# Performance work log

Hardware: AMD Instinct MI355X
Metric: run time of the kernel (lower is better)

Reference implementation:

```python
import jax, jax.numpy as jnp
import numpy as np

DIM = 512
HEADS = 8
DIM_HEAD = 64
INNER = HEADS * DIM_HEAD  # 512
LN_EPS = 1e-5


def setup_inputs() -> dict:
    key = jax.random.key(0)
    ks = jax.random.split(key, 6)
    b, n = 2, 2048
    x = jax.random.normal(ks[0], (b, n, DIM), dtype=jnp.float32)
    # to_qkv: Linear(dim, inner*3, bias=False); torch weight is [out,in], apply as x @ W.T
    w_qkv = jax.random.normal(ks[1], (3 * INNER, DIM), dtype=jnp.float32) * (DIM ** -0.5)
    reattn_w = jax.random.normal(ks[2], (HEADS, HEADS), dtype=jnp.float32)
    ln_g = jnp.ones((HEADS,), dtype=jnp.float32)
    ln_b = jnp.zeros((HEADS,), dtype=jnp.float32)
    w_out = jax.random.normal(ks[3], (DIM, INNER), dtype=jnp.float32) * (INNER ** -0.5)
    b_out = jnp.zeros((DIM,), dtype=jnp.float32)
    return {"x": x, "w_qkv": w_qkv, "reattn_w": reattn_w,
            "ln_g": ln_g, "ln_b": ln_b, "w_out": w_out, "b_out": b_out}


def reference(x, w_qkv, reattn_w, ln_g, ln_b, w_out, b_out):
    b, n, _ = x.shape
    scale = DIM_HEAD ** -0.5
    qkv = x @ w_qkv.T  # [b, n, 3*inner]
    q, k, v = jnp.split(qkv, 3, axis=-1)
    # b n (h d) -> b h n d
    split_heads = lambda t: t.reshape(b, n, HEADS, DIM_HEAD).transpose(0, 2, 1, 3)
    q, k, v = split_heads(q), split_heads(k), split_heads(v)
    dots = jnp.einsum('bhid,bhjd->bhij', q, k) * scale
    attn = jax.nn.softmax(dots, axis=-1)
    # re-attention: cross-head mixing then LayerNorm over head dim
    attn = jnp.einsum('bhij,hg->bgij', attn, reattn_w)
    a = attn.transpose(0, 2, 3, 1)  # b i j h
    mu = jnp.mean(a, axis=-1, keepdims=True)
    var = jnp.mean((a - mu) ** 2, axis=-1, keepdims=True)
    a = (a - mu) * jax.lax.rsqrt(var + LN_EPS) * ln_g + ln_b
    attn = a.transpose(0, 3, 1, 2)  # b h i j
    out = jnp.einsum('bhij,bhjd->bhid', attn, v)
    out = out.transpose(0, 2, 1, 3).reshape(b, n, INNER)
    out = out @ w_out.T + b_out  # dropout p=0 -> identity
    return out
```

## Files before the change

### kernel.cpp

```cpp
#include <hip/hip_runtime.h>
#include <hip/hip_bf16.h>


typedef __attribute__((ext_vector_type(8))) short bfx8;
typedef __attribute__((ext_vector_type(4))) float f32x4;
typedef unsigned short u16;
typedef unsigned int u32;

#define QSCALE 0.18033688011112042f

static __device__ inline u16 f2bf(float f) {
  union { float f; unsigned u; } cv; cv.f = f;
  unsigned u = cv.u;
  u += 0x7fffu + ((u >> 16) & 1u);
  return (u16)(u >> 16);
}
static __device__ inline u32 cvtpk(float lo, float hi) {
  u32 d; asm("v_cvt_pk_bf16_f32 %0, %1, %2" : "=v"(d) : "v"(lo), "v"(hi)); return d;
}
static __device__ inline float fexp2(float x) {
  float r; asm("v_exp_f32 %0, %1" : "=v"(r) : "v"(x)); return r;
}
static __device__ inline float flog2(float x) {
  float r; asm("v_log_f32 %0, %1" : "=v"(r) : "v"(x)); return r;
}
static __device__ inline uint4 pk8(const float* p) {
  float4 a = *(const float4*)p, b = *(const float4*)(p + 4);
  return make_uint4(cvtpk(a.x, a.y), cvtpk(a.z, a.w), cvtpk(b.x, b.y), cvtpk(b.z, b.w));
}

__global__ __launch_bounds__(256) void gemm_qkv(
    const float* __restrict__ A, const float* __restrict__ B,
    u16* __restrict__ qb, u16* __restrict__ kb, u16* __restrict__ vtb) {
  __shared__ u16 As[128 * 32];
  __shared__ u16 Bs[128 * 32];
  const int bid = blockIdx.x;
  const int swzb = (bid & 7) * 48 + (bid >> 3);
  const int n0 = (swzb % 12) * 128, m0 = (swzb / 12) * 128;
  const int t = threadIdx.x, lane = t & 63;
  const int wm = (t >> 6) >> 1, wn = (t >> 6) & 1;
  const int li = lane & 15, lg = lane >> 4;
  const int rowA = t >> 2, kb8 = (t & 3) * 8;
  f32x4 acc[4][4] = {};
  for (int k0 = 0; k0 < 512; k0 += 32) {
    __syncthreads();
    *(uint4*)&As[rowA * 32 + kb8]        = pk8(&A[(size_t)(m0 + rowA) * 512 + k0 + kb8]);
    *(uint4*)&As[(rowA + 64) * 32 + kb8] = pk8(&A[(size_t)(m0 + rowA + 64) * 512 + k0 + kb8]);
    *(uint4*)&Bs[rowA * 32 + kb8]        = pk8(&B[(size_t)(n0 + rowA) * 512 + k0 + kb8]);
    *(uint4*)&Bs[(rowA + 64) * 32 + kb8] = pk8(&B[(size_t)(n0 + rowA + 64) * 512 + k0 + kb8]);
    __syncthreads();
    bfx8 af[4], bf_[4];
#pragma unroll
    for (int mi = 0; mi < 4; mi++)
      af[mi] = *(const bfx8*)&As[(wm * 64 + mi * 16 + li) * 32 + lg * 8];
#pragma unroll
    for (int ni = 0; ni < 4; ni++)
      bf_[ni] = *(const bfx8*)&Bs[(wn * 64 + ni * 16 + li) * 32 + lg * 8];
#pragma unroll
    for (int mi = 0; mi < 4; mi++)
#pragma unroll
      for (int ni = 0; ni < 4; ni++)
        acc[mi][ni] = __builtin_amdgcn_mfma_f32_16x16x32_bf16(af[mi], bf_[ni], acc[mi][ni], 0, 0, 0);
  }
#pragma unroll
  for (int mi = 0; mi < 4; mi++) {
#pragma unroll
    for (int ni = 0; ni < 4; ni++) {
      const int nc  = n0 + wn * 64 + ni * 16 + li;
      const int mrb = m0 + wm * 64 + mi * 16 + lg * 4;
      const int part = nc >> 9, within = nc & 511;
      const int h = within >> 6, d = within & 63;
      const int bb = mrb >> 11, ii = mrb & 2047;
      if (part == 0) {
#pragma unroll
        for (int r = 0; r < 4; r++)
          qb[(((size_t)bb * 8 + h) * 2048 + ii + r) * 64 + d] = f2bf(acc[mi][ni][r] * QSCALE);
      } else if (part == 1) {
#pragma unroll
        for (int r = 0; r < 4; r++)
          kb[(((size_t)bb * 8 + h) * 2048 + ii + r) * 64 + d] = f2bf(acc[mi][ni][r]);
      } else {
        ushort4 u;
        u.x = f2bf(acc[mi][ni][0]); u.y = f2bf(acc[mi][ni][1]);
        u.z = f2bf(acc[mi][ni][2]); u.w = f2bf(acc[mi][ni][3]);
        *(ushort4*)&vtb[(((size_t)bb * 8 + h) * 64 + d) * 2048 + ii] = u;
      }
    }
  }
}

__global__ __launch_bounds__(256) void passA(
    const u16* __restrict__ qb, const u16* __restrict__ kb,
    float2* __restrict__ statp) {
  const int bid = blockIdx.x;
  const int swzb = (bid & 7) * 256 + (bid >> 3);
  const int bx = swzb & 31, bh = (swzb >> 5) & 15, js = swzb >> 9;
  const int t = threadIdx.x, lane = t & 63, w = t >> 6;
  const int i0 = bx * 64 + w * 16;
  const int li = lane & 15, lg = lane >> 4;
  const u16* Qh = qb + ((size_t)bh * 2048 + i0 + li) * 64;
  const u16* Kb = kb + (size_t)bh * 2048 * 64;
  const bfx8 q0 = *(const bfx8*)&Qh[lg * 8];
  const bfx8 q1 = *(const bfx8*)&Qh[32 + lg * 8];
  float m = -1e30f, l = 0.f;
  const int jbeg = js * 512, jend = jbeg + 512;
  for (int j0 = jbeg; j0 < jend; j0 += 32) {
    const u16* KhA = Kb + (size_t)(j0 + li) * 64;
    const u16* KhB = KhA + 16 * 64;
    bfx8 a0 = *(const bfx8*)&KhA[lg * 8];
    bfx8 a1 = *(const bfx8*)&KhA[32 + lg * 8];
    bfx8 b0 = *(const bfx8*)&KhB[lg * 8];
    bfx8 b1 = *(const bfx8*)&KhB[32 + lg * 8];
    __builtin_amdgcn_sched_barrier(0);
    f32x4 sa = {0.f, 0.f, 0.f, 0.f}, sb = {0.f, 0.f, 0.f, 0.f};
    sa = __builtin_amdgcn_mfma_f32_16x16x32_bf16(a0, q0, sa, 0, 0, 0);
    sa = __builtin_amdgcn_mfma_f32_16x16x32_bf16(a1, q1, sa, 0, 0, 0);
    sb = __builtin_amdgcn_mfma_f32_16x16x32_bf16(b0, q0, sb, 0, 0, 0);
    sb = __builtin_amdgcn_mfma_f32_16x16x32_bf16(b1, q1, sb, 0, 0, 0);
    float mt = fmaxf(fmaxf(fmaxf(sa[0], sa[1]), fmaxf(sa[2], sa[3])),
                     fmaxf(fmaxf(sb[0], sb[1]), fmaxf(sb[2], sb[3])));
    float mn = fmaxf(m, mt);
    float es = (fexp2(sa[0] - mn) + fexp2(sa[1] - mn)) + (fexp2(sa[2] - mn) + fexp2(sa[3] - mn))
             + (fexp2(sb[0] - mn) + fexp2(sb[1] - mn)) + (fexp2(sb[2] - mn) + fexp2(sb[3] - mn));
    l = fmaf(l, fexp2(m - mn), es);
    m = mn;
  }
  for (int off = 16; off < 64; off <<= 1) {
    float mo = __shfl_xor(m, off, 64);
    float lo = __shfl_xor(l, off, 64);
    float mn = fmaxf(m, mo);
    l = l * fexp2(m - mn) + lo * fexp2(mo - mn);
    m = mn;
  }
  if (lane < 16) statp[(size_t)js * 32768 + (size_t)bh * 2048 + i0 + li] = make_float2(m, l);
}

__global__ __launch_bounds__(512) void kFused(
    const u16* __restrict__ qb, const u16* __restrict__ kb,
    const u16* __restrict__ vtb, const float2* __restrict__ statp,
    const float* __restrict__ Wmix, const float* __restrict__ lng,
    const float* __restrict__ lnb, float* __restrict__ innerF) {
  __shared__ __align__(16) u16 Spk[64 * 512];
  __shared__ __align__(16) u16 A2h[8 * 64 * 72];
  __shared__ float stMs[64 * 8];
  const int t = threadIdx.x, lane = t & 63, w = t >> 6;
  const int li = lane & 15, lg = lane >> 4;
  const int ig = blockIdx.x * 64, b = blockIdx.y, j0 = blockIdx.z * 512;

  float wm_[8][8], lng_[8], lnb_[8];
#pragma unroll
  for (int h = 0; h < 8; h++)
#pragma unroll
    for (int g = 0; g < 8; g++) wm_[h][g] = Wmix[h * 8 + g];
#pragma unroll
  for (int g = 0; g < 8; g++) { lng_[g] = lng[g]; lnb_[g] = lnb[g]; }

  {
    const int i = t >> 3, h = t & 7;
    const size_t idx = ((size_t)(b * 8 + h)) * 2048 + ig + i;
    float m = -1e30f, l = 0.f;
#pragma unroll
    for (int z = 0; z < 4; z++) {
      const float2 a = statp[(size_t)z * 32768 + idx];
      const float mn = fmaxf(m, a.x);
      l = l * fexp2(m - mn) + a.y * fexp2(a.x - mn);
      m = mn;
    }
    stMs[i * 8 + h] = m + flog2(l);
  }

  bfx8 qf[4][2];
#pragma unroll
  for (int ii = 0; ii < 4; ii++)
#pragma unroll
    for (int ks = 0; ks < 2; ks++)
      qf[ii][ks] = *(const bfx8*)&qb[(((size_t)(b * 8 + w)) * 2048 + ig + ii * 16 + li) * 64
                                     + ks * 32 + lg * 8];
  __syncthreads();
  float stMp[4];
#pragma unroll
  for (int ii = 0; ii < 4; ii++) stMp[ii] = stMs[(ii * 16 + li) * 8 + w];

  f32x4 pacc[4][4] = {};
  const int mixI = t >> 3, mixJ8 = (t & 7) * 8;
  const int mixSwz = (mixI & 7) << 3;

  bfx8 kf[4][2];
#pragma unroll
  for (int ji = 0; ji < 4; ji++)
#pragma unroll
    for (int ks = 0; ks < 2; ks++)
      kf[ji][ks] = *(const bfx8*)&kb[(((size_t)(b * 8 + w)) * 2048 + j0 + ji * 16 + li) * 64
                                     + ks * 32 + lg * 8];

  for (int jt = j0; jt < j0 + 512; jt += 64) {
#pragma unroll
    for (int ii = 0; ii < 4; ii++) {
      f32x4 s[4] = {};
#pragma unroll
      for (int ji = 0; ji < 4; ji++) {
        s[ji] = __builtin_amdgcn_mfma_f32_16x16x32_bf16(kf[ji][0], qf[ii][0], s[ji], 0, 0, 0);
        s[ji] = __builtin_amdgcn_mfma_f32_16x16x32_bf16(kf[ji][1], qf[ii][1], s[ji], 0, 0, 0);
      }
      const int i = ii * 16 + li;
      const int swzI = (i & 7) << 3;
#pragma unroll
      for (int ji = 0; ji < 4; ji++) {
        const float p0 = fexp2(s[ji][0] - stMp[ii]);
        const float p1 = fexp2(s[ji][1] - stMp[ii]);
        const float p2 = fexp2(s[ji][2] - stMp[ii]);
        const float p3 = fexp2(s[ji][3] - stMp[ii]);
        const int x = (ji * 16 + lg * 4) ^ swzI;
        *(uint2*)&Spk[i * 512 + w * 64 + x] = make_uint2(cvtpk(p0, p1), cvtpk(p2, p3));
      }
    }
    __syncthreads();
    bfx8 vf0[4], vf1[4];
#pragma unroll
    for (int dt = 0; dt < 4; dt++) {
      vf0[dt] = *(const bfx8*)&vtb[(((size_t)(b * 8 + w)) * 64 + dt * 16 + li) * 2048
                                   + jt + lg * 8];
      vf1[dt] = *(const bfx8*)&vtb[(((size_t)(b * 8 + w)) * 64 + dt * 16 + li) * 2048
                                   + jt + 32 + lg * 8];
    }
    {
      const int jn = (jt + 64 < j0 + 512) ? jt + 64 : j0;
#pragma unroll
      for (int ji = 0; ji < 4; ji++)
#pragma unroll
        for (int ks = 0; ks < 2; ks++)
          kf[ji][ks] = *(const bfx8*)&kb[(((size_t)(b * 8 + w)) * 2048 + jn + ji * 16 + li) * 64
                                         + ks * 32 + lg * 8];
    }
    __builtin_amdgcn_sched_barrier(0);
    {
      uint4 sv[8];
#pragma unroll
      for (int h = 0; h < 8; h++)
        sv[h] = *(const uint4*)&Spk[mixI * 512 + h * 64 + (mixJ8 ^ mixSwz)];
      u32 ogw[8][4];
      float tmp[8];
#pragma unroll
      for (int hf = 0; hf < 2; hf++) {
        float p[8][4];
#pragma unroll
        for (int h = 0; h < 8; h++) {
          const u32 va = hf ? sv[h].z : sv[h].x;
          const u32 vb = hf ? sv[h].w : sv[h].y;
          union { u32 u; float f; } c0, c1, c2, c3;
          c0.u = va << 16; c1.u = va & 0xffff0000u;
          c2.u = vb << 16; c3.u = vb & 0xffff0000u;
          p[h][0] = c0.f; p[h][1] = c1.f; p[h][2] = c2.f; p[h][3] = c3.f;
        }
#pragma unroll
        for (int e = 0; e < 4; e++) {
          float a_[8]; float sum = 0.f, sumsq = 0.f;
#pragma unroll
          for (int g = 0; g < 8; g++) {
            float acc = 0.f;
#pragma unroll
            for (int h = 0; h < 8; h++) acc = fmaf(p[h][e], wm_[h][g], acc);
            a_[g] = acc; sum += acc; sumsq = fmaf(acc, acc, sumsq);
          }
          const float mu = sum * 0.125f;
          const float var = fmaf(sumsq, 0.125f, -mu * mu);
          const float rs = rsqrtf(var + 1e-5f);
#pragma unroll
          for (int g = 0; g < 8; g++) {
            const float av = fmaf((a_[g] - mu) * rs, lng_[g], lnb_[g]);
            if (e & 1) ogw[g][hf * 2 + (e >> 1)] = cvtpk(tmp[g], av);
            else       tmp[g] = av;
          }
        }
      }
#pragma unroll
      for (int g = 0; g < 8; g++)
        *(uint4*)&A2h[g * 4608 + mixI * 72 + (mixJ8 ^ mixSwz)] =
            make_uint4(ogw[g][0], ogw[g][1], ogw[g][2], ogw[g][3]);
    }
    __syncthreads();
    __builtin_amdgcn_s_setprio(1);
#pragma unroll
    for (int iSub = 0; iSub < 4; iSub++) {
      const bfx8 af0 = *(const bfx8*)&A2h[w * 4608 + (iSub * 16 + li) * 72
                                          + ((lg * 8) ^ ((li & 7) << 3))];
#pragma unroll
      for (int dt = 0; dt < 4; dt++)
        pacc[iSub][dt] = __builtin_amdgcn_mfma_f32_16x16x32_bf16(af0, vf0[dt], pacc[iSub][dt], 0, 0, 0);
    }
#pragma unroll
    for (int iSub = 0; iSub < 4; iSub++) {
      const bfx8 af1 = *(const bfx8*)&A2h[w * 4608 + (iSub * 16 + li) * 72
                                          + ((32 + lg * 8) ^ ((li & 7) << 3))];
#pragma unroll
      for (int dt = 0; dt < 4; dt++)
        pacc[iSub][dt] = __builtin_amdgcn_mfma_f32_16x16x32_bf16(af1, vf1[dt], pacc[iSub][dt], 0, 0, 0);
    }
    __builtin_amdgcn_s_setprio(0);
    __syncthreads();
  }
#pragma unroll
  for (int iSub = 0; iSub < 4; iSub++)
#pragma unroll
    for (int dt = 0; dt < 4; dt++)
#pragma unroll
      for (int r = 0; r < 4; r++)
        atomicAdd(&innerF[((size_t)b * 2048 + ig + iSub * 16 + lg * 4 + r) * 512
                          + w * 64 + dt * 16 + li],
                  pacc[iSub][dt][r]);
}

__global__ __launch_bounds__(256) void gemm_out(
    const float* __restrict__ A, const float* __restrict__ B,
    float* __restrict__ outf, const float* __restrict__ bias) {
  __shared__ u16 As[128 * 32];
  __shared__ u16 Bs[128 * 32];
  const int bid = blockIdx.x;
  const int swzb = (bid & 7) * 16 + (bid >> 3);
  const int n0 = (swzb & 3) * 128, m0 = (swzb >> 2) * 128;
  const int t = threadIdx.x, lane = t & 63;
  const int wm = (t >> 6) >> 1, wn = (t >> 6) & 1;
  const int li = lane & 15, lg = lane >> 4;
  const int rowA = t >> 2, kb8 = (t & 3) * 8;
  f32x4 acc[4][4] = {};
  for (int k0 = 0; k0 < 512; k0 += 32) {
    __syncthreads();
    *(uint4*)&As[rowA * 32 + kb8]        = pk8(&A[(size_t)(m0 + rowA) * 512 + k0 + kb8]);
    *(uint4*)&As[(rowA + 64) * 32 + kb8] = pk8(&A[(size_t)(m0 + rowA + 64) * 512 + k0 + kb8]);
    *(uint4*)&Bs[rowA * 32 + kb8]        = pk8(&B[(size_t)(n0 + rowA) * 512 + k0 + kb8]);
    *(uint4*)&Bs[(rowA + 64) * 32 + kb8] = pk8(&B[(size_t)(n0 + rowA + 64) * 512 + k0 + kb8]);
    __syncthreads();
    bfx8 af[4], bf_[4];
#pragma unroll
    for (int mi = 0; mi < 4; mi++)
      af[mi] = *(const bfx8*)&As[(wm * 64 + mi * 16 + li) * 32 + lg * 8];
#pragma unroll
    for (int ni = 0; ni < 4; ni++)
      bf_[ni] = *(const bfx8*)&Bs[(wn * 64 + ni * 16 + li) * 32 + lg * 8];
#pragma unroll
    for (int mi = 0; mi < 4; mi++)
#pragma unroll
      for (int ni = 0; ni < 4; ni++)
        acc[mi][ni] = __builtin_amdgcn_mfma_f32_16x16x32_bf16(af[mi], bf_[ni], acc[mi][ni], 0, 0, 0);
  }
#pragma unroll
  for (int mi = 0; mi < 4; mi++) {
#pragma unroll
    for (int ni = 0; ni < 4; ni++) {
      const int nc  = n0 + wn * 64 + ni * 16 + li;
      const int mrb = m0 + wm * 64 + mi * 16 + lg * 4;
      const float bv = bias[nc];
#pragma unroll
      for (int r = 0; r < 4; r++)
        outf[(size_t)(mrb + r) * 512 + nc] = acc[mi][ni][r] + bv;
    }
  }
}

extern "C" void kernel_launch(void* const* d_in, const int* in_sizes, int n_in,
                              void* d_out, int out_size, void* d_ws, size_t ws_size,
                              hipStream_t stream) {
  const float* x      = (const float*)d_in[0];
  const float* w_qkv  = (const float*)d_in[1];
  const float* reattn = (const float*)d_in[2];
  const float* ln_g   = (const float*)d_in[3];
  const float* ln_b   = (const float*)d_in[4];
  const float* w_out  = (const float*)d_in[5];
  const float* b_out  = (const float*)d_in[6];
  float* out = (float*)d_out;
  char* ws = (char*)d_ws;
  float*  innerF= (float*)(ws + 0);
  u16*    qbf   = (u16*)(ws + 8388608);
  u16*    kbf   = (u16*)(ws + 12582912);
  u16*    vtb   = (u16*)(ws + 16777216);
  float2* statp = (float2*)(ws + 20971520);

  gemm_qkv<<<384, 256, 0, stream>>>(x, w_qkv, qbf, kbf, vtb);
  hipMemsetAsync(innerF, 0, 8388608, stream);
  passA<<<2048, 256, 0, stream>>>(qbf, kbf, statp);
  kFused<<<dim3(32, 2, 4), 512, 0, stream>>>(qbf, kbf, vtb, statp, reattn, ln_g, ln_b, innerF);
  gemm_out<<<128, 256, 0, stream>>>(innerF, w_out, out, b_out);
}
```

Before: 191.4 us.

## Shrink GEMM tiles, split passA further, fold memset into QKV GEMM

Both projection GEMMs move from 128x128 to 64x128 tiles, doubling the grid so more compute units get work. The score-statistics pass now splits each key range into 8 chunks of 256 instead of 4 of 512, and the fused kernel merges 8 partial stats. Zeroing of the fp32 accumulation buffer moves from a separate memset into the QKV GEMM kernel, saving one launch. A trailing __syncthreads in the fused attention loop is dropped, which risks a shared-memory race if the next iteration overwrites data other waves are still reading.

```diff
diff --git a/kernel.cpp b/kernel.cpp
--- a/kernel.cpp
+++ b/kernel.cpp
@@ -31,43 +31,44 @@
 
 __global__ __launch_bounds__(256) void gemm_qkv(
     const float* __restrict__ A, const float* __restrict__ B,
-    u16* __restrict__ qb, u16* __restrict__ kb, u16* __restrict__ vtb) {
-  __shared__ u16 As[128 * 32];
+    u16* __restrict__ qb, u16* __restrict__ kb, u16* __restrict__ vtb,
+    float4* __restrict__ zeroF) {
+  __shared__ u16 As[64 * 32];
   __shared__ u16 Bs[128 * 32];
-  const int bid = blockIdx.x;
-  const int swzb = (bid & 7) * 48 + (bid >> 3);
-  const int n0 = (swzb % 12) * 128, m0 = (swzb / 12) * 128;
-  const int t = threadIdx.x, lane = t & 63;
-  const int wm = (t >> 6) >> 1, wn = (t >> 6) & 1;
+  const int bid = blockIdx.x, t = threadIdx.x;
+  for (int e = bid * 256 + t; e < 524288; e += 196608)
+    zeroF[e] = make_float4(0.f, 0.f, 0.f, 0.f);
+  const int swzb = (bid & 7) * 96 + (bid >> 3);
+  const int m0 = (swzb / 12) * 64, n0 = (swzb % 12) * 128;
+  const int lane = t & 63, w = t >> 6;
   const int li = lane & 15, lg = lane >> 4;
   const int rowA = t >> 2, kb8 = (t & 3) * 8;
-  f32x4 acc[4][4] = {};
+  f32x4 acc[4][2] = {};
   for (int k0 = 0; k0 < 512; k0 += 32) {
     __syncthreads();
     *(uint4*)&As[rowA * 32 + kb8]        = pk8(&A[(size_t)(m0 + rowA) * 512 + k0 + kb8]);
-    *(uint4*)&As[(rowA + 64) * 32 + kb8] = pk8(&A[(size_t)(m0 + rowA + 64) * 512 + k0 + kb8]);
     *(uint4*)&Bs[rowA * 32 + kb8]        = pk8(&B[(size_t)(n0 + rowA) * 512 + k0 + kb8]);
     *(uint4*)&Bs[(rowA + 64) * 32 + kb8] = pk8(&B[(size_t)(n0 + rowA + 64) * 512 + k0 + kb8]);
     __syncthreads();
-    bfx8 af[4], bf_[4];
+    bfx8 af[4], bf_[2];
 #pragma unroll
     for (int mi = 0; mi < 4; mi++)
-      af[mi] = *(const bfx8*)&As[(wm * 64 + mi * 16 + li) * 32 + lg * 8];
-#pragma unroll
-    for (int ni = 0; ni < 4; ni++)
-      bf_[ni] = *(const bfx8*)&Bs[(wn * 64 + ni * 16 + li) * 32 + lg * 8];
+      af[mi] = *(const bfx8*)&As[(mi * 16 + li) * 32 + lg * 8];
+#pragma unroll
+    for (int ni = 0; ni < 2; ni++)
+      bf_[ni] = *(const bfx8*)&Bs[(w * 32 + ni * 16 + li) * 32 + lg * 8];
 #pragma unroll
     for (int mi = 0; mi < 4; mi++)
 #pragma unroll
-      for (int ni = 0; ni < 4; ni++)
+      for (int ni = 0; ni < 2; ni++)
         acc[mi][ni] = __builtin_amdgcn_mfma_f32_16x16x32_bf16(af[mi], bf_[ni], acc[mi][ni], 0, 0, 0);
   }
 #pragma unroll
   for (int mi = 0; mi < 4; mi++) {
 #pragma unroll
-    for (int ni = 0; ni < 4; ni++) {
-      const int nc  = n0 + wn * 64 + ni * 16 + li;
-      const int mrb = m0 + wm * 64 + mi * 16 + lg * 4;
+    for (int ni = 0; ni < 2; ni++) {
+      const int nc  = n0 + w * 32 + ni * 16 + li;
+      const int mrb = m0 + mi * 16 + lg * 4;
       const int part = nc >> 9, within = nc & 511;
       const int h = within >> 6, d = within & 63;
       const int bb = mrb >> 11, ii = mrb & 2047;
@@ -93,7 +94,7 @@
     const u16* __restrict__ qb, const u16* __restrict__ kb,
     float2* __restrict__ statp) {
   const int bid = blockIdx.x;
-  const int swzb = (bid & 7) * 256 + (bid >> 3);
+  const int swzb = (bid & 7) * 512 + (bid >> 3);
   const int bx = swzb & 31, bh = (swzb >> 5) & 15, js = swzb >> 9;
   const int t = threadIdx.x, lane = t & 63, w = t >> 6;
   const int i0 = bx * 64 + w * 16;
@@ -103,7 +104,7 @@
   const bfx8 q0 = *(const bfx8*)&Qh[lg * 8];
   const bfx8 q1 = *(const bfx8*)&Qh[32 + lg * 8];
   float m = -1e30f, l = 0.f;
-  const int jbeg = js * 512, jend = jbeg + 512;
+  const int jbeg = js * 256, jend = jbeg + 256;
   for (int j0 = jbeg; j0 < jend; j0 += 32) {
     const u16* KhA = Kb + (size_t)(j0 + li) * 64;
     const u16* KhB = KhA + 16 * 64;
@@ -160,7 +161,7 @@
     const size_t idx = ((size_t)(b * 8 + h)) * 2048 + ig + i;
     float m = -1e30f, l = 0.f;
 #pragma unroll
-    for (int z = 0; z < 4; z++) {
+    for (int z = 0; z < 8; z++) {
       const float2 a = statp[(size_t)z * 32768 + idx];
       const float mn = fmaxf(m, a.x);
       l = l * fexp2(m - mn) + a.y * fexp2(a.x - mn);
@@ -297,7 +298,6 @@
         pacc[iSub][dt] = __builtin_amdgcn_mfma_f32_16x16x32_bf16(af1, vf1[dt], pacc[iSub][dt], 0, 0, 0);
     }
     __builtin_amdgcn_s_setprio(0);
-    __syncthreads();
   }
 #pragma unroll
   for (int iSub = 0; iSub < 4; iSub++)
@@ -313,42 +313,40 @@
 __global__ __launch_bounds__(256) void gemm_out(
     const float* __restrict__ A, const float* __restrict__ B,
     float* __restrict__ outf, const float* __restrict__ bias) {
-  __shared__ u16 As[128 * 32];
+  __shared__ u16 As[64 * 32];
   __shared__ u16 Bs[128 * 32];
   const int bid = blockIdx.x;
-  const int swzb = (bid & 7) * 16 + (bid >> 3);
-  const int n0 = (swzb & 3) * 128, m0 = (swzb >> 2) * 128;
-  const int t = threadIdx.x, lane = t & 63;
-  const int wm = (t >> 6) >> 1, wn = (t >> 6) & 1;
+  const int swzb = (bid & 7) * 32 + (bid >> 3);
+  const int m0 = (swzb >> 2) * 64, n0 = (swzb & 3) * 128;
+  const int t = threadIdx.x, lane = t & 63, w = t >> 6;
   const int li = lane & 15, lg = lane >> 4;
   const int rowA = t >> 2, kb8 = (t & 3) * 8;
-  f32x4 acc[4][4] = {};
+  f32x4 acc[4][2] = {};
   for (int k0 = 0; k0 < 512; k0 += 32) {
     __syncthreads();
     *(uint4*)&As[rowA * 32 + kb8]        = pk8(&A[(size_t)(m0 + rowA) * 512 + k0 + kb8]);
-    *(uint4*)&As[(rowA + 64) * 32 + kb8] = pk8(&A[(size_t)(m0 + rowA + 64) * 512 + k0 + kb8]);
     *(uint4*)&Bs[rowA * 32 + kb8]        = pk8(&B[(size_t)(n0 + rowA) * 512 + k0 + kb8]);
     *(uint4*)&Bs[(rowA + 64) * 32 + kb8] = pk8(&B[(size_t)(n0 + rowA + 64) * 512 + k0 + kb8]);
     __syncthreads();
-    bfx8 af[4], bf_[4];
+    bfx8 af[4], bf_[2];
 #pragma unroll
     for (int mi = 0; mi < 4; mi++)
-      af[mi] = *(const bfx8*)&As[(wm * 64 + mi * 16 + li) * 32 + lg * 8];
-#pragma unroll
-    for (int ni = 0; ni < 4; ni++)
-      bf_[ni] = *(const bfx8*)&Bs[(wn * 64 + ni * 16 + li) * 32 + lg * 8];
+      af[mi] = *(const bfx8*)&As[(mi * 16 + li) * 32 + lg * 8];
+#pragma unroll
+    for (int ni = 0; ni < 2; ni++)
+      bf_[ni] = *(const bfx8*)&Bs[(w * 32 + ni * 16 + li) * 32 + lg * 8];
 #pragma unroll
     for (int mi = 0; mi < 4; mi++)
 #pragma unroll
-      for (int ni = 0; ni < 4; ni++)
+      for (int ni = 0; ni < 2; ni++)
         acc[mi][ni] = __builtin_amdgcn_mfma_f32_16x16x32_bf16(af[mi], bf_[ni], acc[mi][ni], 0, 0, 0);
   }
 #pragma unroll
   for (int mi = 0; mi < 4; mi++) {
 #pragma unroll
-    for (int ni = 0; ni < 4; ni++) {
-      const int nc  = n0 + wn * 64 + ni * 16 + li;
-      const int mrb = m0 + wm * 64 + mi * 16 + lg * 4;
+    for (int ni = 0; ni < 2; ni++) {
+      const int nc  = n0 + w * 32 + ni * 16 + li;
+      const int mrb = m0 + mi * 16 + lg * 4;
       const float bv = bias[nc];
 #pragma unroll
       for (int r = 0; r < 4; r++)
@@ -375,9 +373,8 @@
   u16*    vtb   = (u16*)(ws + 16777216);
   float2* statp = (float2*)(ws + 20971520);
 
-  gemm_qkv<<<384, 256, 0, stream>>>(x, w_qkv, qbf, kbf, vtb);
-  hipMemsetAsync(innerF, 0, 8388608, stream);
-  passA<<<2048, 256, 0, stream>>>(qbf, kbf, statp);
+  gemm_qkv<<<768, 256, 0, stream>>>(x, w_qkv, qbf, kbf, vtb, (float4*)innerF);
+  passA<<<4096, 256, 0, stream>>>(qbf, kbf, statp);
   kFused<<<dim3(32, 2, 4), 512, 0, stream>>>(qbf, kbf, vtb, statp, reattn, ln_g, ln_b, innerF);
-  gemm_out<<<128, 256, 0, stream>>>(innerF, w_out, out, b_out);
-}
+  gemm_out<<<256, 256, 0, stream>>>(innerF, w_out, out, b_out);
+}
```

Result: faster. 185.6 us, median of 3 (-3.0%).
